# Performance work log

Hardware: AMD Instinct MI355X
Metric: run time of the kernel (lower is better)

## Reference

```python
import jax, jax.numpy as jnp
import numpy as np

B_, L, DM = 2, 1024, 1024
D_STATE, D_CONV, EXPAND = 16, 4, 2
DI = EXPAND * DM          # 2048 inner dim
DTR = DM // 16            # 64 dt rank


def setup_inputs() -> dict:
    key = jax.random.key(0)
    ks = jax.random.split(key, 16)
    g = lambda k, shp, s: jax.random.normal(k, shp, jnp.float32) * s
    inp = {
        "x": g(ks[0], (B_, L, DM), 1.0),
        "ln_g": jnp.ones((DM,), jnp.float32),
        "ln_b": jnp.zeros((DM,), jnp.float32),
        "in_proj_w": g(ks[1], (2 * DI, DM), (2.0 / (DM + 2 * DI)) ** 0.5),
        "conv_w": g(ks[2], (DI, 1, D_CONV), (2.0 / D_CONV) ** 0.5),
        "conv_b": jnp.zeros((DI,), jnp.float32),
        "dtin_w": g(ks[3], (DTR, DI), (2.0 / (DI + DTR)) ** 0.5),
        "dtin_b": jnp.zeros((DTR,), jnp.float32),
        "dt_w": g(ks[4], (DI, DTR), DTR ** -0.5),
        "dt_b": jnp.log(jnp.expm1(jax.random.uniform(ks[5], (DI,), jnp.float32, 1e-3, 0.1))),  # inverse-softplus of dt in [dt_min, dt_max]
        "B_w": g(ks[6], (D_STATE, DI), DI ** -0.5),
        "C_w": g(ks[7], (D_STATE, DI), DI ** -0.5),
        "A_log": jnp.log(jnp.broadcast_to(jnp.arange(1, D_STATE + 1, dtype=jnp.float32), (DI, D_STATE))),
        "D": jnp.ones((DI,), jnp.float32),
        "out_w": g(ks[8], (DM, DI), (2.0 / (DM + DI)) ** 0.5),
    }
    return inp


def _layernorm(x, g, b, eps=1e-5):
    mu = jnp.mean(x, -1, keepdims=True)
    var = jnp.mean(jnp.square(x - mu), -1, keepdims=True)
    return (x - mu) * jax.lax.rsqrt(var + eps) * g + b


def _selective_scan(u, dt, Bm, Cm, A, Dp):
    # u,dt: (b,l,di); Bm,Cm: (b,l,n); A: (di,n)
    def step(h, inp):
        dt_t, B_t, C_t, u_t = inp  # (b,di),(b,n),(b,n),(b,di)
        dA = jnp.exp(dt_t[..., None] * A)                       # (b,di,n)
        h = h * dA + (dt_t * u_t)[..., None] * B_t[:, None, :]   # (b,di,n)
        y = jnp.einsum("bdn,bn->bd", h, C_t)
        return h, y

    tm = lambda a: jnp.swapaxes(a, 0, 1)  # time-major
    h0 = jnp.zeros((u.shape[0], u.shape[2], A.shape[1]), u.dtype)
    _, ys = jax.lax.scan(step, h0, (tm(dt), tm(Bm), tm(Cm), tm(u)))
    return jnp.swapaxes(ys, 0, 1) + u * Dp  # (b,l,di)


def reference(x, ln_g, ln_b, in_proj_w, conv_w, conv_b, dtin_w, dtin_b,
              dt_w, dt_b, B_w, C_w, A_log, D, out_w):
    residual = x
    xn = _layernorm(x, ln_g, ln_b)
    xz = xn @ in_proj_w.T                       # (b,l,2*di)
    x_proj, z = jnp.split(xz, 2, axis=-1)
    # causal depthwise conv1d (left pad d_conv-1, truncate to seq_len)
    xp = jnp.pad(x_proj, ((0, 0), (D_CONV - 1, 0), (0, 0)))
    x_conv = conv_b
    for k in range(D_CONV):
        x_conv = x_conv + conv_w[:, 0, k] * xp[:, k:k + L, :]
    x_conv = jax.nn.silu(x_conv)
    dt_in = x_conv @ dtin_w.T + dtin_b          # (b,l,dtr)
    dt = jax.nn.softplus(dt_in @ dt_w.T + dt_b) # (b,l,di)
    Bm = x_conv @ B_w.T                         # (b,l,n)
    Cm = x_conv @ C_w.T
    A = -jnp.exp(A_log)                         # (di,n)
    y = _selective_scan(x_conv, dt, Bm, Cm, A, D)
    y = y * jax.nn.silu(z)
    return y @ out_w.T + residual
```

## Files before the change

kernel.cpp:

```cpp
#include <hip/hip_runtime.h>
#include <hip/hip_bf16.h>
#include <cstdint>

#define BL    2
#define LSEQ  1024
#define DMOD  1024
#define DIN   2048
#define NST   16
#define DTRK  64
#define MR    (BL*LSEQ)

#define CCH 32
#define TCH 32
#define KSPLIT 8

typedef __bf16 bf16x8 __attribute__((ext_vector_type(8)));
typedef float  f32x4  __attribute__((ext_vector_type(4)));

#if __has_builtin(__builtin_amdgcn_exp2f)
#define EXP2F(x) __builtin_amdgcn_exp2f(x)
#else
#define EXP2F(x) exp2f(x)
#endif
#define LOG2E 1.4426950408889634f

__device__ __forceinline__ void glds16(const void* g, const void* l) {
    __builtin_amdgcn_global_load_lds(
        (__attribute__((address_space(1))) void*)(uintptr_t)(g),
        (__attribute__((address_space(3))) void*)(uint32_t)(uintptr_t)(l),
        16, 0, 0);
}

__device__ __forceinline__ __bf16 f2b(float f) {
    __hip_bfloat16 t = __float2bfloat16(f);
    return *(__bf16*)&t;
}

template <int MODE, int TM, int TN, int BK>
__global__ __launch_bounds__(256, 3) void gemm_bt(
    const __hip_bfloat16* __restrict__ A, int lda,
    const __hip_bfloat16* __restrict__ Bw, int ldb,
    int M, int N, int Ksl,
    void* __restrict__ e0, void* __restrict__ e1,
    const float* __restrict__ bias, const float* __restrict__ bias2,
    const float* __restrict__ Af)
{
    constexpr bool FUSE = (MODE == 0);
    static_assert(!FUSE || BK == 64, "fused conv epilogue assumes BK=64");
    static_assert(MODE != 2 || BK == 64, "MODE 2 staging assumes BK=64");
    static_assert((MODE != 0 && MODE != 2) || TN == 128, "LDS flush assumes TN=128");
    constexpr int WM = TM / 2, WN = TN / 2;
    constexpr int MT = WM / 16, NT = WN / 16;
    constexpr int C8 = BK / 8;
    constexpr int RPP = 256 / C8;
    constexpr int PA = TM / RPP, PB = TN / RPP;
    __shared__ __align__(16) __hip_bfloat16 sA[2][TM * BK];
    __shared__ __align__(16) __hip_bfloat16 sB[2][TN * BK];
    __shared__ __align__(16) __hip_bfloat16 sH[2][(FUSE ? 16 : 1) * 64];

    auto SW = [](int row) { return (BK == 32) ? ((row >> 1) & 3) : (row & 7); };

    int bx = blockIdx.x, by = blockIdx.y;
    if ((gridDim.y & 7) == 0) {
        const int bid = blockIdx.x + gridDim.x * blockIdx.y;
        const int xcd = bid & 7, s = bid >> 3;
        const int ypx = gridDim.y >> 3;
        const int gx  = ((gridDim.x & 7) == 0) ? 8 : 1;
        const int gsz = gx * ypx;
        const int grp = s / gsz, r = s % gsz;
        bx = grp * gx + (r % gx);
        by = (r / gx) * 8 + xcd;
    }
    const int m0 = by * TM;
    const int n0 = bx * TN;
    const int k0 = blockIdx.z * Ksl;
    const int tid = threadIdx.x;
    const int w = tid >> 6, lane = tid & 63;
    const int wm = (w >> 1) * WM, wn = (w & 1) * WN;
    const int lrow = lane & 15, lq = lane >> 4;

    const int r0 = tid / C8;
    const int q = ((tid % C8) - SW(r0)) & (C8 - 1);
    const __hip_bfloat16* pa[PA];
    const __hip_bfloat16* pb[PB];
    if constexpr (MODE != 2) {
#pragma unroll
        for (int p = 0; p < PA; p++) pa[p] = A + (size_t)(m0 + r0 + RPP * p) * lda + k0 + q * 8;
    }
#pragma unroll
    for (int p = 0; p < PB; p++) pb[p] = Bw + (size_t)(n0 + r0 + RPP * p) * ldb + k0 + q * 8;

    auto stageA2 = [&](int buf, int kb) {
        if constexpr (MODE == 2) {
#pragma unroll
            for (int p = 0; p < PA; p++) {
                const int rr = r0 + RPP * p;
                const float* src = Af + (size_t)(m0 + rr) * 64 + kb * BK + q * 8;
                const float4 f0 = *(const float4*)src;
                const float4 f1 = *(const float4*)(src + 4);
                const float4 b0 = *(const float4*)&bias2[q * 8];
                const float4 b1 = *(const float4*)&bias2[q * 8 + 4];
                bf16x8 o;
                o[0] = f2b(f0.x + b0.x); o[1] = f2b(f0.y + b0.y);
                o[2] = f2b(f0.z + b0.z); o[3] = f2b(f0.w + b0.w);
                o[4] = f2b(f1.x + b1.x); o[5] = f2b(f1.y + b1.y);
                o[6] = f2b(f1.z + b1.z); o[7] = f2b(f1.w + b1.w);
                *(bf16x8*)&sA[buf][(tid + 256 * p) * 8] = o;
            }
        }
    };

    const bool isX = FUSE && (n0 < DIN);
    const __hip_bfloat16* ph = nullptr;
    if (FUSE) {
        const int rh = tid >> 3;
        const int qh = ((tid & 7) - (rh & 7)) & 7;
        ph = A + (size_t)(m0 - 16 + rh) * lda + k0 + qh * 8;
    }

    f32x4 acc[MT][NT];
#pragma unroll
    for (int i = 0; i < MT; i++)
#pragma unroll
        for (int j = 0; j < NT; j++) { acc[i][j][0]=0.f; acc[i][j][1]=0.f; acc[i][j][2]=0.f; acc[i][j][3]=0.f; }
    f32x4 hacc[FUSE ? NT : 1];
    if (FUSE)
#pragma unroll
        for (int j = 0; j < NT; j++) { hacc[j][0]=0.f; hacc[j][1]=0.f; hacc[j][2]=0.f; hacc[j][3]=0.f; }

    const int nk = Ksl / BK;
    if constexpr (MODE == 2) stageA2(0, 0);
    else {
#pragma unroll
        for (int p = 0; p < PA; p++) glds16(pa[p], &sA[0][(tid + 256 * p) * 8]);
    }
#pragma unroll
    for (int p = 0; p < PB; p++) glds16(pb[p], &sB[0][(tid + 256 * p) * 8]);
    if (isX && tid < 128) glds16(ph, &sH[0][tid * 8]);

    for (int kb = 0; kb < nk; ++kb) {
        const int cur = kb & 1, nxt = cur ^ 1;
        __syncthreads();
        if (kb + 1 < nk) {
            if constexpr (MODE == 2) stageA2(nxt, kb + 1);
            else {
#pragma unroll
                for (int p = 0; p < PA; p++) { pa[p] += BK; glds16(pa[p], &sA[nxt][(tid + 256 * p) * 8]); }
            }
#pragma unroll
            for (int p = 0; p < PB; p++) { pb[p] += BK; glds16(pb[p], &sB[nxt][(tid + 256 * p) * 8]); }
            if (isX && tid < 128) { ph += BK; glds16(ph, &sH[nxt][tid * 8]); }
        }
#pragma unroll
        for (int s = 0; s < BK / 32; s++) {
            bf16x8 af[MT], bb[NT];
#pragma unroll
            for (int mt = 0; mt < MT; mt++) {
                const int row = wm + mt * 16 + lrow;
                const int pc = ((s * 4 + lq) + SW(row)) & (C8 - 1);
                af[mt] = *(const bf16x8*)&sA[cur][row * BK + pc * 8];
            }
#pragma unroll
            for (int nt = 0; nt < NT; nt++) {
                const int row = wn + nt * 16 + lrow;
                const int pc = ((s * 4 + lq) + SW(row)) & (C8 - 1);
                bb[nt] = *(const bf16x8*)&sB[cur][row * BK + pc * 8];
            }
#pragma unroll
            for (int mt = 0; mt < MT; mt++)
#pragma unroll
                for (int nt = 0; nt < NT; nt++)
                    acc[mt][nt] = __builtin_amdgcn_mfma_f32_16x16x32_bf16(af[mt], bb[nt], acc[mt][nt], 0, 0, 0);
            if (isX && w < 2) {
                const int pcH = ((s * 4 + lq) + (lrow & 7)) & 7;
                const bf16x8 afh = *(const bf16x8*)&sH[cur][lrow * 64 + pcH * 8];
#pragma unroll
                for (int nt = 0; nt < NT; nt++)
                    hacc[nt] = __builtin_amdgcn_mfma_f32_16x16x32_bf16(afh, bb[nt], hacc[nt], 0, 0, 0);
            }
        }
    }

    if constexpr (MODE == 0) {
        if (isX) {
            __syncthreads();
            __hip_bfloat16* tile = (__hip_bfloat16*)&sB[0][0];
            constexpr int TS = TN + 8;
#pragma unroll
            for (int mt = 0; mt < MT; mt++)
#pragma unroll
                for (int nt = 0; nt < NT; nt++) {
                    const int col = wn + nt * 16 + lrow;
#pragma unroll
                    for (int r = 0; r < 4; r++)
                        tile[(16 + wm + mt * 16 + lq * 4 + r) * TS + col] = __float2bfloat16(acc[mt][nt][r]);
                }
            if (w < 2) {
#pragma unroll
                for (int nt = 0; nt < NT; nt++) {
                    const int col = wn + nt * 16 + lrow;
#pragma unroll
                    for (int r = 0; r < 4; r++)
                        tile[(lq * 4 + r) * TS + col] = __float2bfloat16(hacc[nt][r]);
                }
            }
            __syncthreads();
            const int c2 = (tid & 63) * 2;
            const int rg = tid >> 6;
            const int dg = n0 + c2;
            const float4 wA = *(const float4*)&bias[dg * 4];
            const float4 wB = *(const float4*)&bias[dg * 4 + 4];
            const float cbA = bias2[dg], cbB = bias2[dg + 1];
            const int l0 = m0 & (LSEQ - 1);
            const int rbase = rg * 16;
            float a0, a1, a2, b0, b1, b2;
            if (l0 == 0 && rg == 0) {
                a0 = a1 = a2 = b0 = b1 = b2 = 0.f;
            } else {
                const int hr = 16 + rbase - 3;
                a0 = __bfloat162float(tile[(hr + 0) * TS + c2]);
                b0 = __bfloat162float(tile[(hr + 0) * TS + c2 + 1]);
                a1 = __bfloat162float(tile[(hr + 1) * TS + c2]);
                b1 = __bfloat162float(tile[(hr + 1) * TS + c2 + 1]);
                a2 = __bfloat162float(tile[(hr + 2) * TS + c2]);
                b2 = __bfloat162float(tile[(hr + 2) * TS + c2 + 1]);
            }
            __hip_bfloat16* xcbp = (__hip_bfloat16*)e0;
#pragma unroll 4
            for (int i = 0; i < 16; i++) {
                const int row = rbase + i;
                const float a3 = __bfloat162float(tile[(16 + row) * TS + c2]);
                const float b3 = __bfloat162float(tile[(16 + row) * TS + c2 + 1]);
                float sa = cbA + wA.x * a0 + wA.y * a1 + wA.z * a2 + wA.w * a3;
                float sb = cbB + wB.x * b0 + wB.y * b1 + wB.z * b2 + wB.w * b3;
                sa = sa / (1.f + __expf(-sa));
                sb = sb / (1.f + __expf(-sb));
                __hip_bfloat16 ha = __float2bfloat16(sa), hb = __float2bfloat16(sb);
                ushort2 o;
                o.x = (unsigned short)__hip_bfloat16_raw(ha).x;
                o.y = (unsigned short)__hip_bfloat16_raw(hb).x;
                *(ushort2*)&xcbp[(size_t)(m0 + row) * DIN + dg] = o;
                a0 = a1; a1 = a2; a2 = a3;
                b0 = b1; b1 = b2; b2 = b3;
            }
        } else {
            __syncthreads();
            __hip_bfloat16* tile = (__hip_bfloat16*)&sB[0][0];
            constexpr int TS = TN + 8;
#pragma unroll
            for (int mt = 0; mt < MT; mt++)
#pragma unroll
                for (int nt = 0; nt < NT; nt++) {
                    const int col = wn + nt * 16 + lrow;
#pragma unroll
                    for (int r = 0; r < 4; r++) {
                        const float v = acc[mt][nt][r];
                        const float sv = v / (1.f + __expf(-v));
                        tile[(wm + mt * 16 + lq * 4 + r) * TS + col] = __float2bfloat16(sv);
                    }
                }
            __syncthreads();
            const int rr = tid >> 4, cq = (tid & 15) * 8;
            __hip_bfloat16* gz = (__hip_bfloat16*)e1 + (size_t)m0 * DIN + (n0 - DIN);
#pragma unroll
            for (int p = 0; p < TM / 16; p++)
                *(bf16x8*)(gz + (size_t)(rr + 16 * p) * DIN + cq) =
                    *(const bf16x8*)&tile[(rr + 16 * p) * TS + cq];
        }
        return;
    }
    if constexpr (MODE == 2) {
        __syncthreads();
        __hip_bfloat16* tile = (__hip_bfloat16*)&sB[0][0];
        constexpr int TS = TN + 8;
#pragma unroll
        for (int mt = 0; mt < MT; mt++)
#pragma unroll
            for (int nt = 0; nt < NT; nt++) {
                const int col = wn + nt * 16 + lrow;
                const float bv = bias[n0 + col];
#pragma unroll
                for (int r = 0; r < 4; r++) {
                    const float xx = acc[mt][nt][r] + bv;
                    const float sp = (xx > 20.f) ? xx : log1pf(__expf(xx));
                    tile[(wm + mt * 16 + lq * 4 + r) * TS + col] = __float2bfloat16(sp);
                }
            }
        __syncthreads();
        const int rr = tid >> 4, cq = (tid & 15) * 8;
        __hip_bfloat16* gy = (__hip_bfloat16*)e0 + (size_t)m0 * N + n0;
#pragma unroll
        for (int p = 0; p < TM / 16; p++)
            *(bf16x8*)(gy + (size_t)(rr + 16 * p) * N + cq) =
                *(const bf16x8*)&tile[(rr + 16 * p) * TS + cq];
        return;
    }
#pragma unroll
    for (int mt = 0; mt < MT; mt++) {
#pragma unroll
        for (int nt = 0; nt < NT; nt++) {
            const int gn = n0 + wn + nt * 16 + lrow;
            if (gn >= N) continue;
            const int gmb = m0 + wm + mt * 16 + lq * 4;
#pragma unroll
            for (int r = 0; r < 4; r++) {
                const int gm = gmb + r;
                const float v = acc[mt][nt][r];
                if (MODE == 1) {
                    if (gn < 64)      atomicAdd((float*)e0 + (size_t)gm * 64 + gn, v);
                    else if (gn < 80) atomicAdd((float*)e1 + (size_t)gm * NST + (gn - 64), v);
                    else              atomicAdd((float*)e1 + (size_t)MR * NST + (size_t)gm * NST + (gn - 80), v);
                } else {
                    ((float*)e0)[(size_t)gm * N + gn] = v + ((const float*)e1)[(size_t)gm * N + gn];
                }
            }
        }
    }
}

#define NCVT 1654784
#define NZR  49152
__global__ void prep_kernel(const float* __restrict__ x, const float* __restrict__ ln_g,
                            const float* __restrict__ ln_b,
                            const float* __restrict__ w_in, const float* __restrict__ dtin_w,
                            const float* __restrict__ B_w, const float* __restrict__ C_w,
                            const float* __restrict__ dt_w, const float* __restrict__ out_w,
                            __hip_bfloat16* __restrict__ w1b, __hip_bfloat16* __restrict__ wpb,
                            __hip_bfloat16* __restrict__ dtwb, __hip_bfloat16* __restrict__ owb,
                            __hip_bfloat16* __restrict__ xn, float* __restrict__ zblock)
{
    const int b = blockIdx.x;
    const int tid = threadIdx.x;
    if (b < MR) {
        const float4 v = ((const float4*)(x + (size_t)b * DMOD))[tid];
        float s  = v.x + v.y + v.z + v.w;
        float sq = v.x * v.x + v.y * v.y + v.z * v.z + v.w * v.w;
#pragma unroll
        for (int off = 32; off >= 1; off >>= 1) {
            s  += __shfl_down(s, off, 64);
            sq += __shfl_down(sq, off, 64);
        }
        __shared__ float red[8];
        const int w = tid >> 6, lane = tid & 63;
        if (lane == 0) { red[w] = s; red[4 + w] = sq; }
        __syncthreads();
        s  = red[0] + red[1] + red[2] + red[3];
        sq = red[4] + red[5] + red[6] + red[7];
        const float mean = s * (1.f / DMOD);
        const float rstd = rsqrtf(sq * (1.f / DMOD) - mean * mean + 1e-5f);
        const int col = tid * 4;
        const float vv[4] = {v.x, v.y, v.z, v.w};
#pragma unroll
        for (int i = 0; i < 4; i++)
            xn[(size_t)b * DMOD + col + i] =
                __float2bfloat16((vv[i] - mean) * rstd * ln_g[col + i] + ln_b[col + i]);
        return;
    }
    const int nb = gridDim.x - MR;
    for (int v4 = (b - MR) * 256 + tid; v4 < NCVT + NZR; v4 += nb * 256) {
        if (v4 >= NCVT) {
            float4 z; z.x = z.y = z.z = z.w = 0.f;
            ((float4*)zblock)[v4 - NCVT] = z;
            continue;
        }
        const int i = v4 * 4;
        const float* s; __hip_bfloat16* dk;
        if      (i < 4194304) { s = w_in   + i;             dk = w1b  + i; }
        else if (i < 4325376) { s = dtin_w + (i - 4194304); dk = wpb  + (i - 4194304); }
        else if (i < 4358144) { s = B_w    + (i - 4325376); dk = wpb  + 131072 + (i - 4325376); }
        else if (i < 4390912) { s = C_w    + (i - 4358144); dk = wpb  + 163840 + (i - 4358144); }
        else if (i < 4521984) { s = dt_w   + (i - 4390912); dk = dtwb + (i - 4390912); }
        else                  { s = out_w  + (i - 4521984); dk = owb  + (i - 4521984); }
        const float4 f = *(const float4*)s;
        ushort4 o;
        o.x = (unsigned short)(__hip_bfloat16_raw(__float2bfloat16(f.x)).x);
        o.y = (unsigned short)(__hip_bfloat16_raw(__float2bfloat16(f.y)).x);
        o.z = (unsigned short)(__hip_bfloat16_raw(__float2bfloat16(f.z)).x);
        o.w = (unsigned short)(__hip_bfloat16_raw(__float2bfloat16(f.w)).x);
        *(ushort4*)dk = o;
    }
}


__global__ __launch_bounds__(256) void scan_p1(
    const __hip_bfloat16* __restrict__ dt, const __hip_bfloat16* __restrict__ u,
    const float* __restrict__ Bm, const float* __restrict__ A_log,
    float* __restrict__ Aprod, float* __restrict__ Bacc)
{
    __shared__ float sB[TCH * NST];
    __shared__ __align__(16) __hip_bfloat16 sDT[TCH * 128];
    __shared__ __align__(16) __hip_bfloat16 sU [TCH * 128];
    const int blk = blockIdx.x;
    const int bb = blk / (CCH * 16), c = (blk >> 4) & (CCH - 1), dtile = blk & 15;
    const int tid = threadIdx.x;
    const int nh = tid & 1, dl = tid >> 1;
    const int d = dtile * 128 + dl;
    const int d0 = dtile * 128;
    const int row0 = bb * LSEQ + c * TCH;

    {
        const int r = tid >> 4, cq = (tid & 15) * 8;
        const __hip_bfloat16* gdt = dt + (size_t)row0 * DIN + d0;
        const __hip_bfloat16* gu  = u  + (size_t)row0 * DIN + d0;
#pragma unroll
        for (int p = 0; p < TCH / 16; p++) {
            glds16(gdt + (size_t)(r + 16 * p) * DIN + cq, &sDT[(r + 16 * p) * 128 + cq]);
            glds16(gu  + (size_t)(r + 16 * p) * DIN + cq, &sU [(r + 16 * p) * 128 + cq]);
        }
    }
#pragma unroll
    for (int k = 0; k < (TCH * NST) / 256; k++)
        sB[tid + 256 * k] = Bm[(size_t)row0 * NST + tid + 256 * k];

    float a2[8];
    {
        const float4 al0 = *(const float4*)&A_log[(size_t)d * NST + nh * 8];
        const float4 al1 = *(const float4*)&A_log[(size_t)d * NST + nh * 8 + 4];
        a2[0] = -__expf(al0.x) * LOG2E; a2[1] = -__expf(al0.y) * LOG2E;
        a2[2] = -__expf(al0.z) * LOG2E; a2[3] = -__expf(al0.w) * LOG2E;
        a2[4] = -__expf(al1.x) * LOG2E; a2[5] = -__expf(al1.y) * LOG2E;
        a2[6] = -__expf(al1.z) * LOG2E; a2[7] = -__expf(al1.w) * LOG2E;
    }
    __syncthreads();

    float h[8], Ap[8];
#pragma unroll
    for (int j = 0; j < 8; j++) { h[j] = 0.f; Ap[j] = 1.f; }

#pragma unroll 4
    for (int t = 0; t < TCH; t++) {
        const float dtv = __bfloat162float(sDT[t * 128 + dl]);
        const float uv  = __bfloat162float(sU [t * 128 + dl]);
        const float du = dtv * uv;
        float bv[8];
        *(float4*)&bv[0] = *(const float4*)&sB[t * NST + nh * 8];
        *(float4*)&bv[4] = *(const float4*)&sB[t * NST + nh * 8 + 4];
#pragma unroll
        for (int j = 0; j < 8; j++) {
            const float e = EXP2F(dtv * a2[j]);
            Ap[j] *= e;
            h[j] = h[j] * e + du * bv[j];
        }
    }
    const size_t idx = (((size_t)bb * CCH + c) * DIN + d) * NST + nh * 8;
    *(float4*)&Aprod[idx]     = make_float4(Ap[0], Ap[1], Ap[2], Ap[3]);
    *(float4*)&Aprod[idx + 4] = make_float4(Ap[4], Ap[5], Ap[6], Ap[7]);
    *(float4*)&Bacc[idx]      = make_float4(h[0], h[1], h[2], h[3]);
    *(float4*)&Bacc[idx + 4]  = make_float4(h[4], h[5], h[6], h[7]);
}

__global__ __launch_bounds__(256) void scan_p2(
    const float* __restrict__ Aprod, const float* __restrict__ Bacc,
    float* __restrict__ hstart)
{
    const int i = blockIdx.x * 256 + threadIdx.x;
    const int bb = i >> 15;
    const int dn = i & 32767;
    const size_t base = (((size_t)bb * CCH) << 15) + dn;
    float ap[CCH], bc[CCH];
#pragma unroll
    for (int c = 0; c < CCH; c++) {
        ap[c] = Aprod[base + ((size_t)c << 15)];
        bc[c] = Bacc[base + ((size_t)c << 15)];
    }
    float hs = 0.f;
#pragma unroll
    for (int c = 0; c < CCH; c++) {
        hstart[base + ((size_t)c << 15)] = hs;
        hs = fmaf(ap[c], hs, bc[c]);
    }
}

__global__ __launch_bounds__(256) void scan_p3(
    const __hip_bfloat16* __restrict__ dt, const __hip_bfloat16* __restrict__ u,
    const float* __restrict__ Bm, const float* __restrict__ Cm,
    const float* __restrict__ A_log, const float* __restrict__ Dp,
    const __hip_bfloat16* __restrict__ zs, const float* __restrict__ hstart,
    __hip_bfloat16* __restrict__ y)
{
    __shared__ float sB[TCH * NST], sC[TCH * NST];
    __shared__ __align__(16) __hip_bfloat16 sDT[TCH * 128];
    __shared__ __align__(16) __hip_bfloat16 sU [TCH * 128];
    __shared__ __align__(16) __hip_bfloat16 sZ [TCH * 128];
    __shared__ __align__(16) __hip_bfloat16 sY [TCH * 128];
    const int blk = blockIdx.x;
    const int bb = blk / (CCH * 16), c = (blk >> 4) & (CCH - 1), dtile = blk & 15;
    const int tid = threadIdx.x;
    const int nh = tid & 1, dl = tid >> 1;
    const int d = dtile * 128 + dl;
    const int d0 = dtile * 128;
    const int row0 = bb * LSEQ + c * TCH;

    {
        const int r = tid >> 4, cq = (tid & 15) * 8;
        const __hip_bfloat16* gdt = dt + (size_t)row0 * DIN + d0;
        const __hip_bfloat16* gu  = u  + (size_t)row0 * DIN + d0;
        const __hip_bfloat16* gz  = zs + (size_t)row0 * DIN + d0;
#pragma unroll
        for (int p = 0; p < TCH / 16; p++) {
            glds16(gdt + (size_t)(r + 16 * p) * DIN + cq, &sDT[(r + 16 * p) * 128 + cq]);
            glds16(gu  + (size_t)(r + 16 * p) * DIN + cq, &sU [(r + 16 * p) * 128 + cq]);
            glds16(gz  + (size_t)(r + 16 * p) * DIN + cq, &sZ [(r + 16 * p) * 128 + cq]);
        }
    }
#pragma unroll
    for (int k = 0; k < (TCH * NST) / 256; k++) {
        sB[tid + 256 * k] = Bm[(size_t)row0 * NST + tid + 256 * k];
        sC[tid + 256 * k] = Cm[(size_t)row0 * NST + tid + 256 * k];
    }

    float a2[8];
    {
        const float4 al0 = *(const float4*)&A_log[(size_t)d * NST + nh * 8];
        const float4 al1 = *(const float4*)&A_log[(size_t)d * NST + nh * 8 + 4];
        a2[0] = -__expf(al0.x) * LOG2E; a2[1] = -__expf(al0.y) * LOG2E;
        a2[2] = -__expf(al0.z) * LOG2E; a2[3] = -__expf(al0.w) * LOG2E;
        a2[4] = -__expf(al1.x) * LOG2E; a2[5] = -__expf(al1.y) * LOG2E;
        a2[6] = -__expf(al1.z) * LOG2E; a2[7] = -__expf(al1.w) * LOG2E;
    }
    const float Dd = Dp[d];
    const size_t idx = (((size_t)bb * CCH + c) * DIN + d) * NST + nh * 8;
    float h[8];
    *(float4*)&h[0] = *(const float4*)&hstart[idx];
    *(float4*)&h[4] = *(const float4*)&hstart[idx + 4];
    __syncthreads();

#pragma unroll 4
    for (int t = 0; t < TCH; t++) {
        const float dtv = __bfloat162float(sDT[t * 128 + dl]);
        const float uv  = __bfloat162float(sU [t * 128 + dl]);
        const float du = dtv * uv;
        float bv[8], cv[8];
        *(float4*)&bv[0] = *(const float4*)&sB[t * NST + nh * 8];
        *(float4*)&bv[4] = *(const float4*)&sB[t * NST + nh * 8 + 4];
        *(float4*)&cv[0] = *(const float4*)&sC[t * NST + nh * 8];
        *(float4*)&cv[4] = *(const float4*)&sC[t * NST + nh * 8 + 4];
        float yp = 0.f;
#pragma unroll
        for (int j = 0; j < 8; j++) {
            const float e = EXP2F(dtv * a2[j]);
            h[j] = h[j] * e + du * bv[j];
            yp += h[j] * cv[j];
        }
        yp += __shfl_xor(yp, 1, 64);
        if (nh == 0) {
            const float zv = __bfloat162float(sZ[t * 128 + dl]);
            sY[t * 128 + dl] = __float2bfloat16((yp + uv * Dd) * zv);
        }
    }
    __syncthreads();
    {
        const int r = tid >> 4, cq = (tid & 15) * 8;
        __hip_bfloat16* gy = y + (size_t)row0 * DIN + d0;
#pragma unroll
        for (int p = 0; p < TCH / 16; p++)
            *(bf16x8*)(gy + (size_t)(r + 16 * p) * DIN + cq) =
                *(const bf16x8*)&sY[(r + 16 * p) * 128 + cq];
    }
}

extern "C" void kernel_launch(void* const* d_in, const int* in_sizes, int n_in,
                              void* d_out, int out_size, void* d_ws, size_t ws_size,
                              hipStream_t stream) {
    const float* x      = (const float*)d_in[0];
    const float* ln_g   = (const float*)d_in[1];
    const float* ln_b   = (const float*)d_in[2];
    const float* w_in   = (const float*)d_in[3];
    const float* conv_w = (const float*)d_in[4];
    const float* conv_b = (const float*)d_in[5];
    const float* dtin_w = (const float*)d_in[6];
    const float* dtin_b = (const float*)d_in[7];
    const float* dt_w   = (const float*)d_in[8];
    const float* dt_b   = (const float*)d_in[9];
    const float* B_w    = (const float*)d_in[10];
    const float* C_w    = (const float*)d_in[11];
    const float* A_log  = (const float*)d_in[12];
    const float* Dp     = (const float*)d_in[13];
    const float* out_w  = (const float*)d_in[14];
    float* out = (float*)d_out;

    char* ws = (char*)d_ws;
    auto alloc = [&](size_t bytes) { char* p = ws; ws += (bytes + 255) & ~255ull; return p; };
    __hip_bfloat16* w1b   = (__hip_bfloat16*)alloc((size_t)4096 * 1024 * 2);
    __hip_bfloat16* wpb   = (__hip_bfloat16*)alloc((size_t)96 * 2048 * 2);
    __hip_bfloat16* dtwb  = (__hip_bfloat16*)alloc((size_t)2048 * 64 * 2);
    __hip_bfloat16* owb   = (__hip_bfloat16*)alloc((size_t)1024 * 2048 * 2);
    __hip_bfloat16* xnb   = (__hip_bfloat16*)alloc((size_t)MR * DMOD * 2);
    __hip_bfloat16* zs    = (__hip_bfloat16*)alloc((size_t)MR * DIN * 2);
    __hip_bfloat16* xcb   = (__hip_bfloat16*)alloc((size_t)MR * DIN * 2);
    __hip_bfloat16* dtb   = (__hip_bfloat16*)alloc((size_t)MR * DIN * 2);
    __hip_bfloat16* yb    = (__hip_bfloat16*)alloc((size_t)MR * DIN * 2);
    float*          zblock= (float*)alloc((size_t)196608 * 4);
    float*          Aprod = (float*)alloc((size_t)BL * CCH * DIN * NST * 4);
    float*          Bacc  = (float*)alloc((size_t)BL * CCH * DIN * NST * 4);
    float*          hstart= (float*)alloc((size_t)BL * CCH * DIN * NST * 4);

    float* fdtin = zblock;
    float* Bmf   = zblock + 131072;

    prep_kernel<<<MR + 896, 256, 0, stream>>>(x, ln_g, ln_b, w_in, dtin_w, B_w, C_w, dt_w,
                                              out_w, w1b, wpb, dtwb, owb, xnb, zblock);

    gemm_bt<0, 64, 128, 64><<<dim3(32, 32, 1), 256, 0, stream>>>(
        xnb, 1024, w1b, 1024, MR, 4096, 1024, xcb, zs, conv_w, conv_b, nullptr);

    gemm_bt<1, 64, 96, 64><<<dim3(1, 32, KSPLIT), 256, 0, stream>>>(
        xcb, 2048, wpb, 2048, MR, 96, 2048 / KSPLIT, fdtin, Bmf, nullptr, nullptr, nullptr);

    gemm_bt<2, 64, 128, 64><<<dim3(16, 32, 1), 256, 0, stream>>>(
        nullptr, 0, dtwb, 64, MR, DIN, 64, dtb, nullptr, dt_b, dtin_b, fdtin);

    scan_p1<<<BL * CCH * 16, 256, 0, stream>>>(dtb, xcb, Bmf, A_log, Aprod, Bacc);
    scan_p2<<<BL * DIN * NST / 256, 256, 0, stream>>>(Aprod, Bacc, hstart);
    scan_p3<<<BL * CCH * 16, 256, 0, stream>>>(dtb, xcb, Bmf, Bmf + (size_t)MR * NST,
                                               A_log, Dp, zs, hstart, yb);

    gemm_bt<3, 64, 64, 64><<<dim3(16, 32, 1), 256, 0, stream>>>(
        yb, 2048, owb, 2048, MR, DMOD, 2048, out, (void*)x, nullptr, nullptr, nullptr);
}
```

Before: 223.6 us.

## Fuse three-phase chunked scan into one cooperative kernel with grid syncs

Replaces the three scan kernels (chunk-local scan, cross-chunk prefix, output pass) with one cooperative launch that uses grid-wide syncs between phases. The dt/u/z chunk tiles and B/C are loaded into shared memory once and reused by both the first and third phases, which saves reloading them and removes two kernel launch gaps. It falls back to the original three kernels if the cooperative launch fails. Risks: grid sync overhead, a 1024-block grid that must all be co-resident, and y now written directly to global with strided per-thread stores instead of the staged coalesced writes.

New measurement: 764.6 us. +241.9%, slower.

```diff
diff --git a/kernel.cpp b/kernel.cpp
--- a/kernel.cpp
+++ b/kernel.cpp
@@ -1,6 +1,9 @@
 #include <hip/hip_runtime.h>
 #include <hip/hip_bf16.h>
+#include <hip/hip_cooperative_groups.h>
 #include <cstdint>
+
+namespace cg = cooperative_groups;
 
 #define BL    2
 #define LSEQ  1024
@@ -559,6 +562,139 @@
     }
 }
 
+__global__ __launch_bounds__(256, 4) void scan_fused(
+    const __hip_bfloat16* __restrict__ dt, const __hip_bfloat16* __restrict__ u,
+    const float* __restrict__ Bm, const float* __restrict__ Cm,
+    const float* __restrict__ A_log, const float* __restrict__ Dp,
+    const __hip_bfloat16* __restrict__ zs,
+    float* __restrict__ Aprod, float* __restrict__ Bacc, float* __restrict__ hstart,
+    __hip_bfloat16* __restrict__ y)
+{
+    __shared__ float sB[TCH * NST], sC[TCH * NST];
+    __shared__ __align__(16) __hip_bfloat16 sDT[TCH * 128];
+    __shared__ __align__(16) __hip_bfloat16 sU [TCH * 128];
+    __shared__ __align__(16) __hip_bfloat16 sZ [TCH * 128];
+    const int blk = blockIdx.x;
+    const int bb = blk / (CCH * 16), c = (blk >> 4) & (CCH - 1), dtile = blk & 15;
+    const int tid = threadIdx.x;
+    const int nh = tid & 1, dl = tid >> 1;
+    const int d = dtile * 128 + dl;
+    const int d0 = dtile * 128;
+    const int row0 = bb * LSEQ + c * TCH;
+
+    {
+        const int r = tid >> 4, cq = (tid & 15) * 8;
+        const __hip_bfloat16* gdt = dt + (size_t)row0 * DIN + d0;
+        const __hip_bfloat16* gu  = u  + (size_t)row0 * DIN + d0;
+        const __hip_bfloat16* gz  = zs + (size_t)row0 * DIN + d0;
+#pragma unroll
+        for (int p = 0; p < TCH / 16; p++) {
+            glds16(gdt + (size_t)(r + 16 * p) * DIN + cq, &sDT[(r + 16 * p) * 128 + cq]);
+            glds16(gu  + (size_t)(r + 16 * p) * DIN + cq, &sU [(r + 16 * p) * 128 + cq]);
+            glds16(gz  + (size_t)(r + 16 * p) * DIN + cq, &sZ [(r + 16 * p) * 128 + cq]);
+        }
+    }
+#pragma unroll
+    for (int k = 0; k < (TCH * NST) / 256; k++) {
+        sB[tid + 256 * k] = Bm[(size_t)row0 * NST + tid + 256 * k];
+        sC[tid + 256 * k] = Cm[(size_t)row0 * NST + tid + 256 * k];
+    }
+
+    float a2[8];
+    {
+        const float4 al0 = *(const float4*)&A_log[(size_t)d * NST + nh * 8];
+        const float4 al1 = *(const float4*)&A_log[(size_t)d * NST + nh * 8 + 4];
+        a2[0] = -__expf(al0.x) * LOG2E; a2[1] = -__expf(al0.y) * LOG2E;
+        a2[2] = -__expf(al0.z) * LOG2E; a2[3] = -__expf(al0.w) * LOG2E;
+        a2[4] = -__expf(al1.x) * LOG2E; a2[5] = -__expf(al1.y) * LOG2E;
+        a2[6] = -__expf(al1.z) * LOG2E; a2[7] = -__expf(al1.w) * LOG2E;
+    }
+    const float Dd = Dp[d];
+    const size_t idx = (((size_t)bb * CCH + c) * DIN + d) * NST + nh * 8;
+    __syncthreads();
+
+    {
+        float h[8], Ap[8];
+#pragma unroll
+        for (int j = 0; j < 8; j++) { h[j] = 0.f; Ap[j] = 1.f; }
+#pragma unroll 4
+        for (int t = 0; t < TCH; t++) {
+            const float dtv = __bfloat162float(sDT[t * 128 + dl]);
+            const float uv  = __bfloat162float(sU [t * 128 + dl]);
+            const float du = dtv * uv;
+            float bv[8];
+            *(float4*)&bv[0] = *(const float4*)&sB[t * NST + nh * 8];
+            *(float4*)&bv[4] = *(const float4*)&sB[t * NST + nh * 8 + 4];
+#pragma unroll
+            for (int j = 0; j < 8; j++) {
+                const float e = EXP2F(dtv * a2[j]);
+                Ap[j] *= e;
+                h[j] = h[j] * e + du * bv[j];
+            }
+        }
+        *(float4*)&Aprod[idx]     = make_float4(Ap[0], Ap[1], Ap[2], Ap[3]);
+        *(float4*)&Aprod[idx + 4] = make_float4(Ap[4], Ap[5], Ap[6], Ap[7]);
+        *(float4*)&Bacc[idx]      = make_float4(h[0], h[1], h[2], h[3]);
+        *(float4*)&Bacc[idx + 4]  = make_float4(h[4], h[5], h[6], h[7]);
+    }
+
+    __threadfence();
+    cg::this_grid().sync();
+    __threadfence();
+
+    if (blk < (BL * DIN * NST) / 256) {
+        const int i = blk * 256 + tid;
+        const int pb = i >> 15;
+        const int dn = i & 32767;
+        const size_t base = (((size_t)pb * CCH) << 15) + dn;
+        float ap[CCH], bc[CCH];
+#pragma unroll
+        for (int cc = 0; cc < CCH; cc++) {
+            ap[cc] = Aprod[base + ((size_t)cc << 15)];
+            bc[cc] = Bacc[base + ((size_t)cc << 15)];
+        }
+        float hs = 0.f;
+#pragma unroll
+        for (int cc = 0; cc < CCH; cc++) {
+            hstart[base + ((size_t)cc << 15)] = hs;
+            hs = fmaf(ap[cc], hs, bc[cc]);
+        }
+    }
+
+    __threadfence();
+    cg::this_grid().sync();
+    __threadfence();
+
+    {
+        float h[8];
+        *(float4*)&h[0] = *(const float4*)&hstart[idx];
+        *(float4*)&h[4] = *(const float4*)&hstart[idx + 4];
+#pragma unroll 4
+        for (int t = 0; t < TCH; t++) {
+            const float dtv = __bfloat162float(sDT[t * 128 + dl]);
+            const float uv  = __bfloat162float(sU [t * 128 + dl]);
+            const float du = dtv * uv;
+            float bv[8], cv[8];
+            *(float4*)&bv[0] = *(const float4*)&sB[t * NST + nh * 8];
+            *(float4*)&bv[4] = *(const float4*)&sB[t * NST + nh * 8 + 4];
+            *(float4*)&cv[0] = *(const float4*)&sC[t * NST + nh * 8];
+            *(float4*)&cv[4] = *(const float4*)&sC[t * NST + nh * 8 + 4];
+            float yp = 0.f;
+#pragma unroll
+            for (int j = 0; j < 8; j++) {
+                const float e = EXP2F(dtv * a2[j]);
+                h[j] = h[j] * e + du * bv[j];
+                yp += h[j] * cv[j];
+            }
+            yp += __shfl_xor(yp, 1, 64);
+            if (nh == 0) {
+                const float zv = __bfloat162float(sZ[t * 128 + dl]);
+                y[(size_t)(row0 + t) * DIN + d] = __float2bfloat16((yp + uv * Dd) * zv);
+            }
+        }
+    }
+}
+
 extern "C" void kernel_launch(void* const* d_in, const int* in_sizes, int n_in,
                               void* d_out, int out_size, void* d_ws, size_t ws_size,
                               hipStream_t stream) {
@@ -597,6 +733,7 @@
 
     float* fdtin = zblock;
     float* Bmf   = zblock + 131072;
+    float* Cmf   = Bmf + (size_t)MR * NST;
 
     prep_kernel<<<MR + 896, 256, 0, stream>>>(x, ln_g, ln_b, w_in, dtin_w, B_w, C_w, dt_w,
                                               out_w, w1b, wpb, dtwb, owb, xnb, zblock);
@@ -610,10 +747,23 @@
     gemm_bt<2, 64, 128, 64><<<dim3(16, 32, 1), 256, 0, stream>>>(
         nullptr, 0, dtwb, 64, MR, DIN, 64, dtb, nullptr, dt_b, dtin_b, fdtin);
 
-    scan_p1<<<BL * CCH * 16, 256, 0, stream>>>(dtb, xcb, Bmf, A_log, Aprod, Bacc);
-    scan_p2<<<BL * DIN * NST / 256, 256, 0, stream>>>(Aprod, Bacc, hstart);
-    scan_p3<<<BL * CCH * 16, 256, 0, stream>>>(dtb, xcb, Bmf, Bmf + (size_t)MR * NST,
-                                               A_log, Dp, zs, hstart, yb);
+    {
+        const __hip_bfloat16* dtc = dtb;
+        const __hip_bfloat16* uc  = xcb;
+        const __hip_bfloat16* zc  = zs;
+        void* cargs[] = {(void*)&dtc, (void*)&uc, (void*)&Bmf, (void*)&Cmf,
+                         (void*)&A_log, (void*)&Dp, (void*)&zc,
+                         (void*)&Aprod, (void*)&Bacc, (void*)&hstart, (void*)&yb};
+        hipError_t ce = hipLaunchCooperativeKernel((void*)scan_fused, dim3(BL * CCH * 16),
+                                                   dim3(256), cargs, 0, stream);
+        if (ce != hipSuccess) {
+            (void)hipGetLastError();
+            scan_p1<<<BL * CCH * 16, 256, 0, stream>>>(dtb, xcb, Bmf, A_log, Aprod, Bacc);
+            scan_p2<<<BL * DIN * NST / 256, 256, 0, stream>>>(Aprod, Bacc, hstart);
+            scan_p3<<<BL * CCH * 16, 256, 0, stream>>>(dtb, xcb, Bmf, Cmf,
+                                                       A_log, Dp, zs, hstart, yb);
+        }
+    }
 
     gemm_bt<3, 64, 64, 64><<<dim3(16, 32, 1), 256, 0, stream>>>(
         yb, 2048, owb, 2048, MR, DMOD, 2048, out, (void*)x, nullptr, nullptr, nullptr);
```

## Fuse x_proj projection GEMM into in_proj conv epilogue with atomics

Applied to the files above, without the earlier changes.

Removes the separate split-K GEMM that projected x_conv onto dt_in/B/C. Each in_proj block writes its conv+silu output tile into LDS, multiplies it by the matching 128-column slice of the projection weights using MFMA, and atomically accumulates into the fp32 dt_in/B/C buffers. This saves a kernel launch and a re-read of xcb from global memory. In exchange it issues many fp32 atomics (16 contributors per output element), adds extra syncs and register pressure in the big GEMM, and makes the summation order nondeterministic.

After: 219.3 us. No clear change (-1.9%).

```diff
diff --git a/kernel.cpp b/kernel.cpp
--- a/kernel.cpp
+++ b/kernel.cpp
@@ -12,7 +12,6 @@
 
 #define CCH 32
 #define TCH 32
-#define KSPLIT 8
 
 typedef __bf16 bf16x8 __attribute__((ext_vector_type(8)));
 typedef float  f32x4  __attribute__((ext_vector_type(4)));
@@ -43,7 +42,7 @@
     int M, int N, int Ksl,
     void* __restrict__ e0, void* __restrict__ e1,
     const float* __restrict__ bias, const float* __restrict__ bias2,
-    const float* __restrict__ Af)
+    float* __restrict__ Af)
 {
     constexpr bool FUSE = (MODE == 0);
     static_assert(!FUSE || BK == 64, "fused conv epilogue assumes BK=64");
@@ -225,6 +224,7 @@
                 a2 = __bfloat162float(tile[(hr + 2) * TS + c2]);
                 b2 = __bfloat162float(tile[(hr + 2) * TS + c2 + 1]);
             }
+            __syncthreads();
             __hip_bfloat16* xcbp = (__hip_bfloat16*)e0;
 #pragma unroll 4
             for (int i = 0; i < 16; i++) {
@@ -240,8 +240,52 @@
                 o.x = (unsigned short)__hip_bfloat16_raw(ha).x;
                 o.y = (unsigned short)__hip_bfloat16_raw(hb).x;
                 *(ushort2*)&xcbp[(size_t)(m0 + row) * DIN + dg] = o;
+                *(ushort2*)&tile[(16 + row) * TS + c2] = o;
                 a0 = a1; a1 = a2; a2 = a3;
                 b0 = b1; b1 = b2; b2 = b3;
+            }
+            __syncthreads();
+            {
+                const __hip_bfloat16* wpb2 = Bw + (size_t)4096 * 1024;
+                const int wm2 = (w >> 1) * 32, wn2 = (w & 1) * 48;
+                f32x4 acc2[2][3];
+#pragma unroll
+                for (int mt2 = 0; mt2 < 2; mt2++)
+#pragma unroll
+                    for (int nt2 = 0; nt2 < 3; nt2++) {
+                        acc2[mt2][nt2][0]=0.f; acc2[mt2][nt2][1]=0.f;
+                        acc2[mt2][nt2][2]=0.f; acc2[mt2][nt2][3]=0.f;
+                    }
+#pragma unroll
+                for (int ks = 0; ks < 4; ks++) {
+                    bf16x8 af2[2], bb2[3];
+#pragma unroll
+                    for (int mt2 = 0; mt2 < 2; mt2++)
+                        af2[mt2] = *(const bf16x8*)&tile[(16 + wm2 + mt2 * 16 + lrow) * TS + ks * 32 + lq * 8];
+#pragma unroll
+                    for (int nt2 = 0; nt2 < 3; nt2++)
+                        bb2[nt2] = *(const bf16x8*)&wpb2[(size_t)(wn2 + nt2 * 16 + lrow) * 2048 + n0 + ks * 32 + lq * 8];
+#pragma unroll
+                    for (int mt2 = 0; mt2 < 2; mt2++)
+#pragma unroll
+                        for (int nt2 = 0; nt2 < 3; nt2++)
+                            acc2[mt2][nt2] = __builtin_amdgcn_mfma_f32_16x16x32_bf16(af2[mt2], bb2[nt2], acc2[mt2][nt2], 0, 0, 0);
+                }
+#pragma unroll
+                for (int mt2 = 0; mt2 < 2; mt2++)
+#pragma unroll
+                    for (int nt2 = 0; nt2 < 3; nt2++) {
+                        const int gn = wn2 + nt2 * 16 + lrow;
+                        const int gmb = m0 + wm2 + mt2 * 16 + lq * 4;
+#pragma unroll
+                        for (int r = 0; r < 4; r++) {
+                            const int gm = gmb + r;
+                            const float v = acc2[mt2][nt2][r];
+                            if (gn < 64)      atomicAdd(Af + (size_t)gm * 64 + gn, v);
+                            else if (gn < 80) atomicAdd(Af + 131072 + (size_t)gm * NST + (gn - 64), v);
+                            else              atomicAdd(Af + 163840 + (size_t)gm * NST + (gn - 80), v);
+                        }
+                    }
             }
         } else {
             __syncthreads();
@@ -597,22 +641,20 @@
 
     float* fdtin = zblock;
     float* Bmf   = zblock + 131072;
+    float* Cmf   = Bmf + (size_t)MR * NST;
 
     prep_kernel<<<MR + 896, 256, 0, stream>>>(x, ln_g, ln_b, w_in, dtin_w, B_w, C_w, dt_w,
                                               out_w, w1b, wpb, dtwb, owb, xnb, zblock);
 
     gemm_bt<0, 64, 128, 64><<<dim3(32, 32, 1), 256, 0, stream>>>(
-        xnb, 1024, w1b, 1024, MR, 4096, 1024, xcb, zs, conv_w, conv_b, nullptr);
-
-    gemm_bt<1, 64, 96, 64><<<dim3(1, 32, KSPLIT), 256, 0, stream>>>(
-        xcb, 2048, wpb, 2048, MR, 96, 2048 / KSPLIT, fdtin, Bmf, nullptr, nullptr, nullptr);
+        xnb, 1024, w1b, 1024, MR, 4096, 1024, xcb, zs, conv_w, conv_b, zblock);
 
     gemm_bt<2, 64, 128, 64><<<dim3(16, 32, 1), 256, 0, stream>>>(
         nullptr, 0, dtwb, 64, MR, DIN, 64, dtb, nullptr, dt_b, dtin_b, fdtin);
 
     scan_p1<<<BL * CCH * 16, 256, 0, stream>>>(dtb, xcb, Bmf, A_log, Aprod, Bacc);
     scan_p2<<<BL * DIN * NST / 256, 256, 0, stream>>>(Aprod, Bacc, hstart);
-    scan_p3<<<BL * CCH * 16, 256, 0, stream>>>(dtb, xcb, Bmf, Bmf + (size_t)MR * NST,
+    scan_p3<<<BL * CCH * 16, 256, 0, stream>>>(dtb, xcb, Bmf, Cmf,
                                                A_log, Dp, zs, hstart, yb);
 
     gemm_bt<3, 64, 64, 64><<<dim3(16, 32, 1), 256, 0, stream>>>(
```
